# Optimization experiments

Hardware: AMD Instinct MI355X
Metric: run time of the kernel (lower is better)

The kernel has to match this reference:

```python
import jax, jax.numpy as jnp
import numpy as np

HIDDEN = 2048
HEADS = 16
HEAD_DIM = HIDDEN // HEADS  # 128


def setup_inputs() -> dict:
    key = jax.random.key(0)
    ks = jax.random.split(key, 9)
    B, S = 2, 2048
    x = jax.random.normal(ks[0], (B, S, HIDDEN), dtype=jnp.float32)
    scale = 1.0 / np.sqrt(HIDDEN)
    Wq = jax.random.normal(ks[1], (HIDDEN, HIDDEN), dtype=jnp.float32) * scale
    Wk = jax.random.normal(ks[2], (HIDDEN, HIDDEN), dtype=jnp.float32) * scale
    Wv = jax.random.normal(ks[3], (HIDDEN, HIDDEN), dtype=jnp.float32) * scale
    Wo = jax.random.normal(ks[4], (HIDDEN, HIDDEN), dtype=jnp.float32) * scale
    bq = jnp.zeros((HIDDEN,), dtype=jnp.float32)
    bk = jnp.zeros((HIDDEN,), dtype=jnp.float32)
    bv = jnp.zeros((HIDDEN,), dtype=jnp.float32)
    bo = jnp.zeros((HIDDEN,), dtype=jnp.float32)
    return {"x": x, "Wq": Wq, "bq": bq, "Wk": Wk, "bk": bk,
            "Wv": Wv, "bv": bv, "Wo": Wo, "bo": bo}


def reference(x, Wq, bq, Wk, bk, Wv, bv, Wo, bo):
    B, S, H = x.shape
    nh, hd = HEADS, HEAD_DIM
    # projections: Linear stores W as [out, in], applies x @ W.T + b
    q = (x @ Wq.T + bq).reshape(B, S, nh, hd).transpose(0, 2, 1, 3)  # [B,nh,S,hd]
    k = (x @ Wk.T + bk).reshape(B, S, nh, hd).transpose(0, 2, 1, 3)
    v = (x @ Wv.T + bv).reshape(B, S, nh, hd).transpose(0, 2, 1, 3)
    scores = jnp.einsum("bhqd,bhkd->bhqk", q, k) / np.sqrt(hd)  # [B,nh,S,S]
    causal = jnp.tril(jnp.ones((S, S), dtype=bool))
    scores = jnp.where(causal[None, None], scores, -jnp.inf)
    probs = jax.nn.softmax(scores, axis=-1)
    attn = jnp.einsum("bhqk,bhkd->bhqd", probs, v)  # [B,nh,S,hd]
    y = attn.transpose(0, 2, 1, 3).reshape(B, S, H)
    return y @ Wo.T + bo
```

## Files before the change

### kernel.cpp

```cpp
#include <hip/hip_runtime.h>

#define HIDDEN 2048
#define NH 16
#define HD 128
#define BATCH 2
#define SEQ 2048

typedef __attribute__((ext_vector_type(8))) short short8;
typedef __attribute__((ext_vector_type(4))) float floatx4;

__device__ inline unsigned short f2bf(float f) {
  union { float f; unsigned int u; } x; x.f = f;
  unsigned int r = x.u + 0x7fffu + ((x.u >> 16) & 1u);
  return (unsigned short)(r >> 16);
}
__device__ inline unsigned int pkbf(float a, float b) {
  return (unsigned int)f2bf(a) | ((unsigned int)f2bf(b) << 16);
}

__device__ inline void async_cp16(const void* g, void* l) {
  __builtin_amdgcn_global_load_lds(
      (const __attribute__((address_space(1))) unsigned int*)g,
      (__attribute__((address_space(3))) unsigned int*)l, 16, 0, 0);
}

__global__ __launch_bounds__(256) void cvt_kernel(const float* __restrict__ in,
                                                  unsigned short* __restrict__ out,
                                                  int n) {
  int i = (blockIdx.x * 256 + threadIdx.x) * 4;
  if (i + 3 < n) {
    float4 v = *reinterpret_cast<const float4*>(in + i);
    ushort4 o;
    o.x = f2bf(v.x); o.y = f2bf(v.y); o.z = f2bf(v.z); o.w = f2bf(v.w);
    *reinterpret_cast<ushort4*>(out + i) = o;
  }
}

struct QkvPtrs {
  const unsigned short* W[3];
  const float* b[3];
  unsigned short* oq[3];
  float oscale[3];
};

template<int MODE>
__global__ __launch_bounds__(256, 4) void gemm_nt(const unsigned short* __restrict__ A,
                                                  QkvPtrs P,
                                                  float* __restrict__ outF) {
  __shared__ __align__(16) unsigned short As[2][4096];
  __shared__ __align__(16) unsigned short Bs[2][4096];
  const int t = threadIdx.x;
  const int lane = t & 63;
  const int w = t >> 6;
  const int wr = w >> 1, wc = w & 1;

  const int nwg = gridDim.x;
  int bid = blockIdx.x;
  int Wi = (bid & 7) * (nwg >> 3) + (bid >> 3);
  const int bx = Wi & 31;
  const int by = Wi >> 5;
  const int wsel = (MODE == 0) ? (by >> 4) : 0;
  const int row0 = bx * 128;
  const int col0 = (by & 15) * 128;

  const unsigned short* Bw = P.W[wsel];
  const float* bias = P.b[wsel];

  floatx4 acc[4][4] = {};

#pragma unroll
  for (int cc = 0; cc < 2; ++cc) {
    int c = t + cc * 256;
    int k8 = c >> 7, r = c & 127;
    async_cp16(A + (size_t)(row0 + r) * 2048 + k8 * 8, &As[0][c * 8]);
    async_cp16(Bw + (size_t)(col0 + r) * 2048 + k8 * 8, &Bs[0][c * 8]);
  }
  __syncthreads();

  int buf = 0;
  for (int kt = 0; kt < 64; ++kt) {
    if (kt < 63) {
      const int kb = (kt + 1) * 32;
#pragma unroll
      for (int cc = 0; cc < 2; ++cc) {
        int c = t + cc * 256;
        int k8 = c >> 7, r = c & 127;
        async_cp16(A + (size_t)(row0 + r) * 2048 + kb + k8 * 8, &As[buf ^ 1][c * 8]);
        async_cp16(Bw + (size_t)(col0 + r) * 2048 + kb + k8 * 8, &Bs[buf ^ 1][c * 8]);
      }
    }
    short8 af[4], bf[4];
#pragma unroll
    for (int m = 0; m < 4; ++m)
      af[m] = *(const short8*)&As[buf][(lane >> 4) * 1024 + (wr * 64 + m * 16 + (lane & 15)) * 8];
#pragma unroll
    for (int n = 0; n < 4; ++n)
      bf[n] = *(const short8*)&Bs[buf][(lane >> 4) * 1024 + (wc * 64 + n * 16 + (lane & 15)) * 8];
#pragma unroll
    for (int m = 0; m < 4; ++m)
#pragma unroll
      for (int n = 0; n < 4; ++n)
        acc[m][n] = __builtin_amdgcn_mfma_f32_16x16x32_bf16(af[m], bf[n], acc[m][n], 0, 0, 0);
    __syncthreads();
    buf ^= 1;
  }

  const float osc = P.oscale[wsel];
#pragma unroll
  for (int m = 0; m < 4; ++m) {
#pragma unroll
    for (int n = 0; n < 4; ++n) {
      int gcol = col0 + wc * 64 + n * 16 + (lane & 15);
      float bv = bias[gcol];
#pragma unroll
      for (int r = 0; r < 4; ++r) {
        int grow = row0 + wr * 64 + m * 16 + (lane >> 4) * 4 + r;
        float v = acc[m][n][r] + bv;
        if (MODE == 1) {
          outF[(size_t)grow * 2048 + gcol] = v;
        } else {
          int bb = grow >> 11;
          int ss = grow & 2047;
          int hh = gcol >> 7;
          int dd = gcol & 127;
          P.oq[wsel][(((size_t)bb * NH + hh) * SEQ + ss) * HD + dd] = f2bf(v * osc);
        }
      }
    }
  }
}

__global__ __launch_bounds__(256) void attn_kernel(const unsigned short* __restrict__ Q,
                                                   const unsigned short* __restrict__ Kg,
                                                   const unsigned short* __restrict__ Vg,
                                                   unsigned short* __restrict__ O) {
  __shared__ __align__(16) unsigned short Ks[2][16 * 64 * 8];
  __shared__ __align__(16) unsigned short VT[2][8 * 128 * 8];

  const int t = threadIdx.x;
  const int lane = t & 63;
  const int w = t >> 6;
  const int g = lane >> 4;
  const int l15 = lane & 15;

  int gid = blockIdx.x;
  int Wi = (gid < 256) ? gid : 767 - gid;
  const int bx = Wi & 15;
  const int bh = Wi >> 4;
  const int q0 = bx * 128;
  const int bb = bh >> 4;
  const int hh = bh & 15;

  const unsigned short* Qb = Q + (size_t)bh * SEQ * HD;
  const unsigned short* Kb = Kg + (size_t)bh * SEQ * HD;
  const unsigned short* Vb = Vg + (size_t)bh * SEQ * HD;

  const int qw = q0 + w * 32;

  short8 bq[2][4];
#pragma unroll
  for (int qh = 0; qh < 2; ++qh)
#pragma unroll
    for (int kb = 0; kb < 4; ++kb)
      bq[qh][kb] = *(const short8*)(Qb + (size_t)(qw + qh * 16 + l15) * HD + kb * 32 + g * 8);

  floatx4 acc[2][8] = {};
  float mrun[2] = {-1e30f, -1e30f};
  float lrun[2] = {0.f, 0.f};

  short8 vreg[4];
  const int vkv = (t >> 4) * 2;
  const int vd0 = (t & 15) * 8;

  const int ntiles = (q0 >> 6) + 2;

  {
#pragma unroll
    for (int cc = 0; cc < 4; ++cc) {
      int c = t + cc * 256;
      int k8 = c >> 6, s = c & 63;
      int kvs = ((s >> 5) << 5) + (((s >> 2) & 3) << 3) + (((s >> 4) & 1) << 2) + (s & 3);
      async_cp16(Kb + (size_t)kvs * HD + k8 * 8, &Ks[0][c * 8]);
    }
#pragma unroll
    for (int cc = 0; cc < 2; ++cc) {
      vreg[cc * 2]     = *(const short8*)(Vb + (size_t)(vkv + cc * 32) * HD + vd0);
      vreg[cc * 2 + 1] = *(const short8*)(Vb + (size_t)(vkv + cc * 32 + 1) * HD + vd0);
    }
#pragma unroll
    for (int cc = 0; cc < 2; ++cc) {
      int kv = vkv + cc * 32;
      int row = kv >> 3;
#pragma unroll
      for (int j = 0; j < 8; ++j) {
        int d = vd0 + j;
        int dp = d ^ (((d >> 3) ^ row) & 7);
        unsigned int u = (unsigned short)vreg[cc * 2][j] |
                         ((unsigned int)(unsigned short)vreg[cc * 2 + 1][j] << 16);
        *(unsigned int*)&VT[0][(row * 128 + dp) * 8 + (kv & 7)] = u;
      }
    }
    __syncthreads();
  }

  for (int tk = 0; tk < ntiles; ++tk) {
    const int buf = tk & 1;
    const int k0 = tk * 64;
    const bool pf = (tk + 1 < ntiles);

    if (pf) {
      const int kn = k0 + 64;
#pragma unroll
      for (int cc = 0; cc < 4; ++cc) {
        int c = t + cc * 256;
        int k8 = c >> 6, s = c & 63;
        int kvs = ((s >> 5) << 5) + (((s >> 2) & 3) << 3) + (((s >> 4) & 1) << 2) + (s & 3);
        async_cp16(Kb + (size_t)(kn + kvs) * HD + k8 * 8, &Ks[buf ^ 1][c * 8]);
      }
#pragma unroll
      for (int cc = 0; cc < 2; ++cc) {
        vreg[cc * 2]     = *(const short8*)(Vb + (size_t)(kn + vkv + cc * 32) * HD + vd0);
        vreg[cc * 2 + 1] = *(const short8*)(Vb + (size_t)(kn + vkv + cc * 32 + 1) * HD + vd0);
      }
    }

    floatx4 sv[4][2];
#pragma unroll
    for (int kvh = 0; kvh < 4; ++kvh) {
      sv[kvh][0] = (floatx4){0.f, 0.f, 0.f, 0.f};
      sv[kvh][1] = (floatx4){0.f, 0.f, 0.f, 0.f};
#pragma unroll
      for (int kb = 0; kb < 4; ++kb) {
        short8 ak = *(const short8*)&Ks[buf][((kb * 4 + g) * 64 + kvh * 16 + l15) * 8];
        sv[kvh][0] = __builtin_amdgcn_mfma_f32_16x16x32_bf16(ak, bq[0][kb], sv[kvh][0], 0, 0, 0);
        sv[kvh][1] = __builtin_amdgcn_mfma_f32_16x16x32_bf16(ak, bq[1][kb], sv[kvh][1], 0, 0, 0);
      }
    }

    if (k0 + 63 > qw) {
#pragma unroll
      for (int kvh = 0; kvh < 4; ++kvh)
#pragma unroll
        for (int qh = 0; qh < 2; ++qh)
#pragma unroll
          for (int r = 0; r < 4; ++r) {
            int kvg = k0 + ((kvh >> 1) << 5) + g * 8 + ((kvh & 1) << 2) + r;
            int qg = qw + qh * 16 + l15;
            if (kvg > qg) sv[kvh][qh][r] = -1e30f;
          }
    }

#pragma unroll
    for (int qh = 0; qh < 2; ++qh) {
      float mt = sv[0][qh][0];
#pragma unroll
      for (int kvh = 0; kvh < 4; ++kvh)
#pragma unroll
        for (int r = 0; r < 4; ++r)
          mt = fmaxf(mt, sv[kvh][qh][r]);
      mt = fmaxf(mt, __shfl_xor(mt, 16, 64));
      mt = fmaxf(mt, __shfl_xor(mt, 32, 64));
      if (__any(mt > mrun[qh] + 8.0f)) {
        float mnew = fmaxf(mrun[qh], mt);
        float f = __expf(mrun[qh] - mnew);
        mrun[qh] = mnew;
        lrun[qh] *= f;
        float fr[4];
#pragma unroll
        for (int r = 0; r < 4; ++r)
          fr[r] = __shfl(f, (lane & 48) + 4 * g + r, 64);
#pragma unroll
        for (int db = 0; db < 8; ++db)
#pragma unroll
          for (int r = 0; r < 4; ++r)
            acc[qh][db][r] *= fr[r];
      }
      float m = mrun[qh];
      float ssum = 0.f;
#pragma unroll
      for (int kvh = 0; kvh < 4; ++kvh)
#pragma unroll
        for (int r = 0; r < 4; ++r) {
          float p = __expf(sv[kvh][qh][r] - m);
          sv[kvh][qh][r] = p;
          ssum += p;
        }
      ssum += __shfl_xor(ssum, 16, 64);
      ssum += __shfl_xor(ssum, 32, 64);
      lrun[qh] += ssum;
    }

#pragma unroll
    for (int kh = 0; kh < 2; ++kh) {
      union { short8 s8; unsigned int u[4]; } p0, p1;
      p0.u[0] = pkbf(sv[2 * kh][0][0], sv[2 * kh][0][1]);
      p0.u[1] = pkbf(sv[2 * kh][0][2], sv[2 * kh][0][3]);
      p0.u[2] = pkbf(sv[2 * kh + 1][0][0], sv[2 * kh + 1][0][1]);
      p0.u[3] = pkbf(sv[2 * kh + 1][0][2], sv[2 * kh + 1][0][3]);
      p1.u[0] = pkbf(sv[2 * kh][1][0], sv[2 * kh][1][1]);
      p1.u[1] = pkbf(sv[2 * kh][1][2], sv[2 * kh][1][3]);
      p1.u[2] = pkbf(sv[2 * kh + 1][1][0], sv[2 * kh + 1][1][1]);
      p1.u[3] = pkbf(sv[2 * kh + 1][1][2], sv[2 * kh + 1][1][3]);
      int row = kh * 4 + g;
#pragma unroll
      for (int db = 0; db < 8; ++db) {
        int d = db * 16 + l15;
        int dp = d ^ (((d >> 3) ^ row) & 7);
        short8 bv = *(const short8*)&VT[buf][(row * 128 + dp) * 8];
        acc[0][db] = __builtin_amdgcn_mfma_f32_16x16x32_bf16(p0.s8, bv, acc[0][db], 0, 0, 0);
        acc[1][db] = __builtin_amdgcn_mfma_f32_16x16x32_bf16(p1.s8, bv, acc[1][db], 0, 0, 0);
      }
    }

    if (pf) {
#pragma unroll
      for (int cc = 0; cc < 2; ++cc) {
        int kv = vkv + cc * 32;
        int row = kv >> 3;
#pragma unroll
        for (int j = 0; j < 8; ++j) {
          int d = vd0 + j;
          int dp = d ^ (((d >> 3) ^ row) & 7);
          unsigned int u = (unsigned short)vreg[cc * 2][j] |
                           ((unsigned int)(unsigned short)vreg[cc * 2 + 1][j] << 16);
          *(unsigned int*)&VT[buf ^ 1][(row * 128 + dp) * 8 + (kv & 7)] = u;
        }
      }
      __syncthreads();
    }
  }

#pragma unroll
  for (int qh = 0; qh < 2; ++qh) {
    float inv = 1.0f / lrun[qh];
    float ir[4];
#pragma unroll
    for (int r = 0; r < 4; ++r)
      ir[r] = __shfl(inv, (lane & 48) + 4 * g + r, 64);
#pragma unroll
    for (int r = 0; r < 4; ++r) {
      int qg = qw + qh * 16 + 4 * g + r;
      size_t base = ((size_t)bb * SEQ + qg) * HIDDEN + hh * HD;
#pragma unroll
      for (int db = 0; db < 8; ++db)
        O[base + db * 16 + l15] = f2bf(acc[qh][db][r] * ir[r]);
    }
  }
}

extern "C" void kernel_launch(void* const* d_in, const int* in_sizes, int n_in,
                              void* d_out, int out_size, void* d_ws, size_t ws_size,
                              hipStream_t stream) {
  (void)in_sizes; (void)n_in; (void)out_size;
  const float* x  = (const float*)d_in[0];
  const float* Wq = (const float*)d_in[1];
  const float* bq = (const float*)d_in[2];
  const float* Wk = (const float*)d_in[3];
  const float* bk = (const float*)d_in[4];
  const float* Wv = (const float*)d_in[5];
  const float* bv = (const float*)d_in[6];
  const float* Wo = (const float*)d_in[7];
  const float* bo = (const float*)d_in[8];
  float* out = (float*)d_out;

  const float qscale = 0.08838834764831845f;
  char* ws = (char*)d_ws;
  dim3 blk(256);
  const bool fused = ws_size >= 92274688ull;

  if (fused) {
    unsigned short* xbf = (unsigned short*)ws;
    unsigned short* W0  = (unsigned short*)(ws + 16777216);
    unsigned short* W1  = (unsigned short*)(ws + 25165824);
    unsigned short* W2  = (unsigned short*)(ws + 33554432);
    unsigned short* Qbf = (unsigned short*)(ws + 41943040);
    unsigned short* Kbf = (unsigned short*)(ws + 58720256);
    unsigned short* Vbf = (unsigned short*)(ws + 75497472);

    cvt_kernel<<<8192, blk, 0, stream>>>(x, xbf, BATCH * SEQ * HIDDEN);
    cvt_kernel<<<4096, blk, 0, stream>>>(Wq, W0, HIDDEN * HIDDEN);
    cvt_kernel<<<4096, blk, 0, stream>>>(Wk, W1, HIDDEN * HIDDEN);
    cvt_kernel<<<4096, blk, 0, stream>>>(Wv, W2, HIDDEN * HIDDEN);

    QkvPtrs Pq;
    Pq.W[0] = W0;  Pq.W[1] = W1;  Pq.W[2] = W2;
    Pq.b[0] = bq;  Pq.b[1] = bk;  Pq.b[2] = bv;
    Pq.oq[0] = Qbf; Pq.oq[1] = Kbf; Pq.oq[2] = Vbf;
    Pq.oscale[0] = qscale; Pq.oscale[1] = 1.0f; Pq.oscale[2] = 1.0f;
    gemm_nt<0><<<1536, blk, 0, stream>>>(xbf, Pq, nullptr);

    attn_kernel<<<512, blk, 0, stream>>>(Qbf, Kbf, Vbf, xbf);

    cvt_kernel<<<4096, blk, 0, stream>>>(Wo, W0, HIDDEN * HIDDEN);
    QkvPtrs Po;
    Po.W[0] = W0; Po.W[1] = W0; Po.W[2] = W0;
    Po.b[0] = bo; Po.b[1] = bo; Po.b[2] = bo;
    Po.oq[0] = nullptr; Po.oq[1] = nullptr; Po.oq[2] = nullptr;
    Po.oscale[0] = 1.0f; Po.oscale[1] = 1.0f; Po.oscale[2] = 1.0f;
    gemm_nt<1><<<512, blk, 0, stream>>>(xbf, Po, out);
  } else {
    unsigned short* xbf = (unsigned short*)ws;
    unsigned short* Wbf = (unsigned short*)(ws + 16777216);
    unsigned short* Qbf = (unsigned short*)(ws + 25165824);
    unsigned short* Kbf = (unsigned short*)(ws + 41943040);
    unsigned short* Vbf = (unsigned short*)(ws + 58720256);

    cvt_kernel<<<8192, blk, 0, stream>>>(x, xbf, BATCH * SEQ * HIDDEN);

    const float* biases[3] = {bq, bk, bv};
    const float* wsrc[3] = {Wq, Wk, Wv};
    unsigned short* outs[3] = {Qbf, Kbf, Vbf};
    float oscales[3] = {qscale, 1.0f, 1.0f};
    for (int i = 0; i < 3; ++i) {
      cvt_kernel<<<4096, blk, 0, stream>>>(wsrc[i], Wbf, HIDDEN * HIDDEN);
      QkvPtrs Pp;
      Pp.W[0] = Wbf; Pp.W[1] = Wbf; Pp.W[2] = Wbf;
      Pp.b[0] = biases[i]; Pp.b[1] = biases[i]; Pp.b[2] = biases[i];
      Pp.oq[0] = outs[i]; Pp.oq[1] = outs[i]; Pp.oq[2] = outs[i];
      Pp.oscale[0] = oscales[i]; Pp.oscale[1] = oscales[i]; Pp.oscale[2] = oscales[i];
      gemm_nt<0><<<512, blk, 0, stream>>>(xbf, Pp, nullptr);
    }

    attn_kernel<<<512, blk, 0, stream>>>(Qbf, Kbf, Vbf, xbf);

    cvt_kernel<<<4096, blk, 0, stream>>>(Wo, Wbf, HIDDEN * HIDDEN);
    QkvPtrs Po;
    Po.W[0] = Wbf; Po.W[1] = Wbf; Po.W[2] = Wbf;
    Po.b[0] = bo; Po.b[1] = bo; Po.b[2] = bo;
    Po.oq[0] = nullptr; Po.oq[1] = nullptr; Po.oq[2] = nullptr;
    Po.oscale[0] = 1.0f; Po.oscale[1] = 1.0f; Po.oscale[2] = 1.0f;
    gemm_nt<1><<<512, blk, 0, stream>>>(xbf, Po, out);
  }
}
```

Baseline: 600.9 us.

## Enlarge GEMM tiles to 256x128 with 512 threads and K-step 64

The projection GEMM now uses 512-thread blocks covering 256-row by 128-column tiles with a 64-wide K slice per stage, halving the loop trip count and the number of barriers. Each A/B load is reused across more MFMAs per block, which cuts global traffic per flop. In exchange, LDS use per block roughly triples (96KB double-buffered), so fewer blocks fit per CU and the grid is halved, which may leave CUs underfilled on the Wo GEMM (256 blocks).

```diff
diff --git a/kernel.cpp b/kernel.cpp
--- a/kernel.cpp
+++ b/kernel.cpp
@@ -44,24 +44,26 @@
 };
 
 template<int MODE>
-__global__ __launch_bounds__(256, 4) void gemm_nt(const unsigned short* __restrict__ A,
+__global__ __launch_bounds__(512, 2) void gemm_nt(const unsigned short* __restrict__ A,
                                                   QkvPtrs P,
                                                   float* __restrict__ outF) {
-  __shared__ __align__(16) unsigned short As[2][4096];
-  __shared__ __align__(16) unsigned short Bs[2][4096];
+  __shared__ __align__(16) unsigned short As[2][16384];
+  __shared__ __align__(16) unsigned short Bs[2][8192];
   const int t = threadIdx.x;
   const int lane = t & 63;
   const int w = t >> 6;
   const int wr = w >> 1, wc = w & 1;
+  const int g = lane >> 4;
+  const int l15 = lane & 15;
 
   const int nwg = gridDim.x;
   int bid = blockIdx.x;
   int Wi = (bid & 7) * (nwg >> 3) + (bid >> 3);
-  const int bx = Wi & 31;
-  const int by = Wi >> 5;
-  const int wsel = (MODE == 0) ? (by >> 4) : 0;
-  const int row0 = bx * 128;
-  const int col0 = (by & 15) * 128;
+  const int bx = Wi & 15;
+  const int byy = Wi >> 4;
+  const int wsel = (MODE == 0) ? (byy >> 4) : 0;
+  const int row0 = bx * 256;
+  const int col0 = (MODE == 0) ? ((byy & 15) * 128) : (byy * 128);
 
   const unsigned short* Bw = P.W[wsel];
   const float* bias = P.b[wsel];
@@ -69,38 +71,54 @@
   floatx4 acc[4][4] = {};
 
 #pragma unroll
-  for (int cc = 0; cc < 2; ++cc) {
-    int c = t + cc * 256;
-    int k8 = c >> 7, r = c & 127;
-    async_cp16(A + (size_t)(row0 + r) * 2048 + k8 * 8, &As[0][c * 8]);
-    async_cp16(Bw + (size_t)(col0 + r) * 2048 + k8 * 8, &Bs[0][c * 8]);
+  for (int i = 0; i < 4; ++i) {
+    int c = t + i * 512;
+    async_cp16(A + (size_t)(row0 + (c & 255)) * 2048 + (c >> 8) * 8, &As[0][c * 8]);
+  }
+#pragma unroll
+  for (int i = 0; i < 2; ++i) {
+    int c = t + i * 512;
+    async_cp16(Bw + (size_t)(col0 + (c & 127)) * 2048 + (c >> 7) * 8, &Bs[0][c * 8]);
   }
   __syncthreads();
 
   int buf = 0;
-  for (int kt = 0; kt < 64; ++kt) {
-    if (kt < 63) {
-      const int kb = (kt + 1) * 32;
-#pragma unroll
-      for (int cc = 0; cc < 2; ++cc) {
-        int c = t + cc * 256;
-        int k8 = c >> 7, r = c & 127;
-        async_cp16(A + (size_t)(row0 + r) * 2048 + kb + k8 * 8, &As[buf ^ 1][c * 8]);
-        async_cp16(Bw + (size_t)(col0 + r) * 2048 + kb + k8 * 8, &Bs[buf ^ 1][c * 8]);
-      }
-    }
-    short8 af[4], bf[4];
-#pragma unroll
-    for (int m = 0; m < 4; ++m)
-      af[m] = *(const short8*)&As[buf][(lane >> 4) * 1024 + (wr * 64 + m * 16 + (lane & 15)) * 8];
-#pragma unroll
-    for (int n = 0; n < 4; ++n)
-      bf[n] = *(const short8*)&Bs[buf][(lane >> 4) * 1024 + (wc * 64 + n * 16 + (lane & 15)) * 8];
-#pragma unroll
-    for (int m = 0; m < 4; ++m)
+  for (int kt = 0; kt < 32; ++kt) {
+    if (kt < 31) {
+      const int kb = (kt + 1) * 64;
+#pragma unroll
+      for (int i = 0; i < 4; ++i) {
+        int c = t + i * 512;
+        async_cp16(A + (size_t)(row0 + (c & 255)) * 2048 + kb + (c >> 8) * 8,
+                   &As[buf ^ 1][c * 8]);
+      }
+#pragma unroll
+      for (int i = 0; i < 2; ++i) {
+        int c = t + i * 512;
+        async_cp16(Bw + (size_t)(col0 + (c & 127)) * 2048 + kb + (c >> 7) * 8,
+                   &Bs[buf ^ 1][c * 8]);
+      }
+    }
+    short8 af[2][4], bf[2][4];
+#pragma unroll
+    for (int ks = 0; ks < 2; ++ks) {
+#pragma unroll
+      for (int m = 0; m < 4; ++m)
+        af[ks][m] = *(const short8*)
+            &As[buf][((ks * 4 + g) * 256 + wr * 64 + m * 16 + l15) * 8];
 #pragma unroll
       for (int n = 0; n < 4; ++n)
-        acc[m][n] = __builtin_amdgcn_mfma_f32_16x16x32_bf16(af[m], bf[n], acc[m][n], 0, 0, 0);
+        bf[ks][n] = *(const short8*)
+            &Bs[buf][((ks * 4 + g) * 128 + wc * 64 + n * 16 + l15) * 8];
+    }
+#pragma unroll
+    for (int ks = 0; ks < 2; ++ks)
+#pragma unroll
+      for (int m = 0; m < 4; ++m)
+#pragma unroll
+        for (int n = 0; n < 4; ++n)
+          acc[m][n] = __builtin_amdgcn_mfma_f32_16x16x32_bf16(af[ks][m], bf[ks][n],
+                                                              acc[m][n], 0, 0, 0);
     __syncthreads();
     buf ^= 1;
   }
@@ -110,11 +128,11 @@
   for (int m = 0; m < 4; ++m) {
 #pragma unroll
     for (int n = 0; n < 4; ++n) {
-      int gcol = col0 + wc * 64 + n * 16 + (lane & 15);
+      int gcol = col0 + wc * 64 + n * 16 + l15;
       float bv = bias[gcol];
 #pragma unroll
       for (int r = 0; r < 4; ++r) {
-        int grow = row0 + wr * 64 + m * 16 + (lane >> 4) * 4 + r;
+        int grow = row0 + wr * 64 + m * 16 + g * 4 + r;
         float v = acc[m][n][r] + bv;
         if (MODE == 1) {
           outF[(size_t)grow * 2048 + gcol] = v;
@@ -366,6 +384,7 @@
   const float qscale = 0.08838834764831845f;
   char* ws = (char*)d_ws;
   dim3 blk(256);
+  dim3 gblk(512);
   const bool fused = ws_size >= 92274688ull;
 
   if (fused) {
@@ -387,7 +406,7 @@
     Pq.b[0] = bq;  Pq.b[1] = bk;  Pq.b[2] = bv;
     Pq.oq[0] = Qbf; Pq.oq[1] = Kbf; Pq.oq[2] = Vbf;
     Pq.oscale[0] = qscale; Pq.oscale[1] = 1.0f; Pq.oscale[2] = 1.0f;
-    gemm_nt<0><<<1536, blk, 0, stream>>>(xbf, Pq, nullptr);
+    gemm_nt<0><<<768, gblk, 0, stream>>>(xbf, Pq, nullptr);
 
     attn_kernel<<<512, blk, 0, stream>>>(Qbf, Kbf, Vbf, xbf);
 
@@ -397,7 +416,7 @@
     Po.b[0] = bo; Po.b[1] = bo; Po.b[2] = bo;
     Po.oq[0] = nullptr; Po.oq[1] = nullptr; Po.oq[2] = nullptr;
     Po.oscale[0] = 1.0f; Po.oscale[1] = 1.0f; Po.oscale[2] = 1.0f;
-    gemm_nt<1><<<512, blk, 0, stream>>>(xbf, Po, out);
+    gemm_nt<1><<<256, gblk, 0, stream>>>(xbf, Po, out);
   } else {
     unsigned short* xbf = (unsigned short*)ws;
     unsigned short* Wbf = (unsigned short*)(ws + 16777216);
@@ -418,7 +437,7 @@
       Pp.b[0] = biases[i]; Pp.b[1] = biases[i]; Pp.b[2] = biases[i];
       Pp.oq[0] = outs[i]; Pp.oq[1] = outs[i]; Pp.oq[2] = outs[i];
       Pp.oscale[0] = oscales[i]; Pp.oscale[1] = oscales[i]; Pp.oscale[2] = oscales[i];
-      gemm_nt<0><<<512, blk, 0, stream>>>(xbf, Pp, nullptr);
+      gemm_nt<0><<<256, gblk, 0, stream>>>(xbf, Pp, nullptr);
     }
 
     attn_kernel<<<512, blk, 0, stream>>>(Qbf, Kbf, Vbf, xbf);
@@ -429,6 +448,6 @@
     Po.b[0] = bo; Po.b[1] = bo; Po.b[2] = bo;
     Po.oq[0] = nullptr; Po.oq[1] = nullptr; Po.oq[2] = nullptr;
     Po.oscale[0] = 1.0f; Po.oscale[1] = 1.0f; Po.oscale[2] = 1.0f;
-    gemm_nt<1><<<512, blk, 0, stream>>>(xbf, Po, out);
-  }
-}
+    gemm_nt<1><<<256, gblk, 0, stream>>>(xbf, Po, out);
+  }
+}
```

Result: slower. 620.7 us (+3.3%).
